# Optimization experiments

Hardware: AMD Instinct MI355X
Metric: run time of the kernel (lower is better)

Reference implementation:

```python
import jax, jax.numpy as jnp
import numpy as np

VOCAB = 100000
EMB = 100
HID = 100
CTX_LEN = 60          # must equal MAX_DESC_LEN for linear_1 to fit
FACT_LEN = 20
DESC_LEN = 60


def setup_inputs() -> dict:
    key = jax.random.key(0)
    ks = jax.random.split(key, 12)
    s = 0.05
    context = jax.random.randint(ks[0], (CTX_LEN, FACT_LEN), 1, VOCAB)
    fact_lengths = jax.random.randint(ks[1], (CTX_LEN,), 1, FACT_LEN)
    description = jax.random.randint(ks[2], (DESC_LEN,), 1, VOCAB)
    emb_ctx = jax.random.normal(ks[3], (VOCAB, EMB), jnp.float32) * s
    emb_ctx = emb_ctx.at[0].set(0.0)  # padding_idx=0
    emb_dec = jax.random.normal(ks[4], (VOCAB, EMB), jnp.float32) * s
    emb_dec = emb_dec.at[0].set(0.0)
    w1 = jax.random.normal(ks[5], (HID, CTX_LEN * HID), jnp.float32) * s
    b1 = jax.random.normal(ks[6], (HID,), jnp.float32) * s
    w_ih = jax.random.normal(ks[7], (3 * HID, EMB), jnp.float32) * s
    w_hh = jax.random.normal(ks[8], (3 * HID, HID), jnp.float32) * s
    b_ih = jax.random.normal(ks[9], (3 * HID,), jnp.float32) * s
    b_hh = jax.random.normal(ks[10], (3 * HID,), jnp.float32) * s
    w_out = jax.random.normal(ks[11], (VOCAB, HID), jnp.float32) * s
    b_out = jnp.zeros((VOCAB,), jnp.float32)
    return {"context": context, "fact_lengths": fact_lengths, "description": description,
            "emb_ctx": emb_ctx, "emb_dec": emb_dec, "w1": w1, "b1": b1,
            "w_ih": w_ih, "w_hh": w_hh, "b_ih": b_ih, "b_hh": b_hh,
            "w_out": w_out, "b_out": b_out}


def _forward(context, description, emb_ctx, emb_dec, w1, b1,
             w_ih, w_hh, b_ih, b_hh, w_out, b_out):
    # ---- InputModule: embed + positional fact encoder ----
    emb = emb_ctx[context]                       # [CTX_LEN, FACT_LEN, EMB]
    slen, elen = FACT_LEN, EMB
    s = jnp.arange(slen, dtype=jnp.float32) / (slen - 1)   # [slen]
    e = jnp.arange(elen, dtype=jnp.float32) / (elen - 1)   # [elen]
    l = 1.0 - s[:, None] - e[None, :] * (1.0 - 2.0 * s[:, None])  # [slen, elen]
    facts = jnp.sum(emb * l[None], axis=1)       # [CTX_LEN, EMB]

    # ---- initial decoder hidden from flattened facts ----
    h0 = facts.reshape(1, -1) @ w1.T + b1        # [1, HID]

    x0 = emb_dec[1][None, :]                     # SOS token embedding [1, EMB]

    def step(carry, tok):
        h, x = carry
        gi = x @ w_ih.T + b_ih                   # [1, 3H]
        gh = h @ w_hh.T + b_hh
        i_r, i_z, i_n = jnp.split(gi, 3, axis=-1)
        h_r, h_z, h_n = jnp.split(gh, 3, axis=-1)
        r = jax.nn.sigmoid(i_r + h_r)
        z = jax.nn.sigmoid(i_z + h_z)
        n = jnp.tanh(i_n + r * h_n)
        h_new = (1.0 - z) * n + z * h            # [1, HID]
        logits = h_new @ w_out.T + b_out         # [1, VOCAB]
        logp = jax.nn.log_softmax(logits, axis=-1)
        loss_t = -logp[0, tok]                   # NLLLoss, batch 1
        x_next = emb_dec[tok][None, :]           # teacher forcing
        return (h_new, x_next), loss_t

    (_, _), losses = jax.lax.scan(step, (h0, x0), description)
    return jnp.sum(losses).reshape(1)            # matches torch FloatTensor([.])


def reference(context, fact_lengths, description, emb_ctx, emb_dec, w1, b1,
              w_ih, w_hh, b_ih, b_hh, w_out, b_out):
    # fact_lengths is unused by the original forward (PositionalFactEncoder ignores it)
    return _forward(context, description, emb_ctx, emb_dec, w1, b1,
                    w_ih, w_hh, b_ih, b_hh, w_out, b_out)
```

## Files before the change

kernel.cpp:

```cpp
#include <hip/hip_runtime.h>
#include <hip/hip_bf16.h>
#include <math.h>

#define VOCAB 100000
#define EMB 100
#define HID 100
#define CTX_LEN 60
#define FACT_LEN 20
#define DESC_LEN 60
#define NCHUNK (VOCAB / 16)
#define GRID_B 224
#define NWAVES_T 892
#define CPW 8

#define WS_H0    64
#define WS_GI    192
#define WS_H     18192
#define WS_MS    24256

typedef __attribute__((ext_vector_type(8))) short short8;
typedef __attribute__((ext_vector_type(4))) float f32x4;

static __device__ __forceinline__ unsigned short f2bf(float f) {
    union { float f; unsigned u; } x; x.f = f;
    unsigned r = (x.u + 0x7FFFu + ((x.u >> 16) & 1u)) >> 16;
    return (unsigned short)r;
}

static __device__ __forceinline__ void release_flag(float* ws, int idx) {
    __builtin_amdgcn_fence(__ATOMIC_RELEASE, "agent");
    __hip_atomic_store((unsigned*)ws + idx, 1u, __ATOMIC_RELAXED, __HIP_MEMORY_SCOPE_AGENT);
}
static __device__ __forceinline__ void wait_flag(const float* ws, int idx) {
    while (__hip_atomic_load((const unsigned*)ws + idx, __ATOMIC_RELAXED,
                             __HIP_MEMORY_SCOPE_AGENT) == 0u)
        __builtin_amdgcn_s_sleep(16);
    __builtin_amdgcn_fence(__ATOMIC_ACQUIRE, "agent");
}

__global__ __launch_bounds__(320) void kA(const int* __restrict__ context,
                                          const int* __restrict__ desc,
                                          const float* __restrict__ emb_ctx,
                                          const float* __restrict__ emb_dec,
                                          const float* __restrict__ w1,
                                          const float* __restrict__ b1,
                                          const float* __restrict__ w_ih,
                                          const float* __restrict__ b_ih,
                                          float* __restrict__ ws,
                                          float* __restrict__ out) {
    const int b = blockIdx.x, tid = threadIdx.x;
    if (b < 100) {
        __shared__ int toks[1200];
        __shared__ float facts[6000];
        __shared__ float red[320];
        for (int i = tid; i < 1200; i += 320) toks[i] = context[i];
        __syncthreads();
        for (int idx = tid; idx < 6000; idx += 320) {
            int fb = idx / 100, e = idx - fb * 100;
            float ef = e * (1.f / 99.f);
            float acc = 0.f;
            #pragma unroll
            for (int s = 0; s < 20; s++) {
                float sf = s * (1.f / 19.f);
                float l = 1.f - sf - ef * (1.f - 2.f * sf);
                acc = fmaf(emb_ctx[toks[fb * 20 + s] * 100 + e], l, acc);
            }
            facts[idx] = acc;
        }
        __syncthreads();
        const float* wr = w1 + b * 6000;
        float p = 0.f;
        for (int k = tid; k < 6000; k += 320) p = fmaf(facts[k], wr[k], p);
        red[tid] = p; __syncthreads();
        if (tid < 64) red[tid] += red[256 + tid];
        __syncthreads();
        for (int st = 128; st > 0; st >>= 1) {
            if (tid < st) red[tid] += red[tid + st];
            __syncthreads();
        }
        if (tid == 0) ws[WS_H0 + b] = red[0] + b1[b];
    } else {
        const int t = b - 100;
        const int tok = (t == 0) ? 1 : desc[t - 1];
        __shared__ float xs[100];
        if (tid < 100) xs[tid] = emb_dec[tok * 100 + tid];
        __syncthreads();
        if (tid < 300) {
            float p = b_ih[tid];
            const float* wr = w_ih + tid * 100;
            #pragma unroll 4
            for (int k = 0; k < 100; k++) p = fmaf(wr[k], xs[k], p);
            ws[WS_GI + t * 300 + tid] = p;
        }
        if (b == 100) {
            if (tid >= 304 && tid < 308) ((unsigned*)ws)[(tid - 304) * 16] = 0u;
            if (tid == 319) out[0] = 0.f;
        }
    }
}

__global__ __launch_bounds__(256, 1) void kB(const float* __restrict__ w_hh,
                                             const float* __restrict__ b_hh,
                                             const float* __restrict__ w_out,
                                             const float* __restrict__ b_out,
                                             float* __restrict__ ws) {
    __shared__ __align__(16) float smem[18128];
    const int b = blockIdx.x, tid = threadIdx.x;
    const int lane = tid & 63, wave = tid >> 6;
    const int q = lane >> 4, n = lane & 15;

    if (b == 0) {
        float* gi_lds = smem;
        unsigned short (*h_bf)[128] = (unsigned short (*)[128])(smem + 18000);
        const int L = lane & 31;
        const int j = wave * 32 + L;
        const bool gate_lane = (lane < 32) && (j < 100);

        short8 bfr[3][2][4];
        #pragma unroll
        for (int s = 0; s < 3; s++) {
            #pragma unroll
            for (int c = 0; c < 2; c++) {
                const int jrow = wave * 32 + c * 16 + n;
                const float* wr = w_hh + (s * 100 + jrow) * 100;
                #pragma unroll
                for (int kt = 0; kt < 4; kt++) {
                    int k0 = kt * 32 + q * 8;
                    float va[8];
                    #pragma unroll
                    for (int jj = 0; jj < 8; jj++) va[jj] = 0.f;
                    if (jrow < 100) {
                        if (k0 + 4 <= 100) {
                            float4 a = *(const float4*)(wr + k0);
                            va[0] = a.x; va[1] = a.y; va[2] = a.z; va[3] = a.w;
                        }
                        if (k0 + 8 <= 100) {
                            float4 a = *(const float4*)(wr + k0 + 4);
                            va[4] = a.x; va[5] = a.y; va[6] = a.z; va[7] = a.w;
                        }
                    }
                    short8 f;
                    #pragma unroll
                    for (int jj = 0; jj < 8; jj++) f[jj] = (short)f2bf(va[jj]);
                    bfr[s][c][kt] = f;
                }
            }
        }

        {
            const float4* src = (const float4*)(ws + WS_GI);
            float4* dst = (float4*)gi_lds;
            for (int k = tid; k < 4500; k += 256) dst[k] = src[k];
        }

        float hreg = 0.f, bh0 = 0.f, bh1 = 0.f, bh2 = 0.f;
        if (gate_lane) {
            hreg = ws[WS_H0 + j];
            bh0 = b_hh[j]; bh1 = b_hh[100 + j]; bh2 = b_hh[200 + j];
        }
        if (tid < 128) {
            h_bf[0][tid] = (tid < 100) ? f2bf(ws[WS_H0 + tid]) : (unsigned short)0;
            h_bf[1][tid] = 0;
        }
        __syncthreads();

        const int js = (j < 100) ? j : 0;
        for (int t = 0; t < 60; t++) {
            const int rb = t & 1;
            float gir = gi_lds[t * 300 + js];
            float giz = gi_lds[t * 300 + 100 + js];
            float gin = gi_lds[t * 300 + 200 + js];

            short8 afr[4];
            #pragma unroll
            for (int kt = 0; kt < 4; kt++)
                afr[kt] = *(const short8*)&h_bf[rb][kt * 32 + q * 8];

            f32x4 acc[3][2];
            #pragma unroll
            for (int s = 0; s < 3; s++) {
                #pragma unroll
                for (int c = 0; c < 2; c++) {
                    f32x4 a = {0.f, 0.f, 0.f, 0.f};
                    a = __builtin_amdgcn_mfma_f32_16x16x32_bf16(afr[0], bfr[s][c][0], a, 0, 0, 0);
                    a = __builtin_amdgcn_mfma_f32_16x16x32_bf16(afr[1], bfr[s][c][1], a, 0, 0, 0);
                    a = __builtin_amdgcn_mfma_f32_16x16x32_bf16(afr[2], bfr[s][c][2], a, 0, 0, 0);
                    a = __builtin_amdgcn_mfma_f32_16x16x32_bf16(afr[3], bfr[s][c][3], a, 0, 0, 0);
                    acc[s][c] = a;
                }
            }

            if (gate_lane) {
                const int cc = L >> 4;
                float ghr = (cc ? acc[0][1][0] : acc[0][0][0]) + bh0;
                float ghz = (cc ? acc[1][1][0] : acc[1][0][0]) + bh1;
                float ghn = (cc ? acc[2][1][0] : acc[2][0][0]) + bh2;
                float r = 1.f / (1.f + __expf(-(gir + ghr)));
                float z = 1.f / (1.f + __expf(-(giz + ghz)));
                float a2 = fmaf(r, ghn, gin);
                float tt = __expf(-2.f * fabsf(a2));
                float nn = copysignf((1.f - tt) / (1.f + tt), a2);
                hreg = (1.f - z) * nn + z * hreg;
                h_bf[rb ^ 1][j] = f2bf(hreg);
                ws[WS_H + t * 100 + j] = hreg;
            }
            __syncthreads();
            if (t == 15 || t == 31 || t == 47 || t == 59) {
                if (tid == 0) release_flag(ws, (t >> 4) * 16);
            }
        }
        return;
    }

    const int gw = (b - 1) * 4 + wave;
    short8 bw[CPW][4];
    #pragma unroll
    for (int k = 0; k < CPW; k++) {
        int c = gw + k * NWAVES_T;
        if (c < NCHUNK) {
            const float* wr = w_out + (c * 16 + n) * 100;
            #pragma unroll
            for (int kt = 0; kt < 4; kt++) {
                int k0 = kt * 32 + q * 8;
                float va[8];
                #pragma unroll
                for (int jj = 0; jj < 8; jj++) va[jj] = 0.f;
                if (k0 + 4 <= 100) {
                    float4 a = *(const float4*)(wr + k0);
                    va[0] = a.x; va[1] = a.y; va[2] = a.z; va[3] = a.w;
                }
                if (k0 + 8 <= 100) {
                    float4 a = *(const float4*)(wr + k0 + 4);
                    va[4] = a.x; va[5] = a.y; va[6] = a.z; va[7] = a.w;
                }
                short8 f;
                #pragma unroll
                for (int jj = 0; jj < 8; jj++) f[jj] = (short)f2bf(va[jj]);
                bw[k][kt] = f;
            }
        }
    }

    const float* H = ws + WS_H;
    const int k_base = q * 8;
    float mS[16], sS[16];
    #pragma unroll
    for (int i = 0; i < 16; i++) { mS[i] = -3.0e38f; sS[i] = 0.f; }

    #pragma unroll
    for (int p = 0; p < 4; p++) {
        if (tid == 0) wait_flag(ws, p * 16);
        __syncthreads();

        short8 afr[4];
        const int m = p * 16 + n;
        #pragma unroll
        for (int kt = 0; kt < 4; kt++) {
            int k0 = kt * 32 + k_base;
            float va[8];
            #pragma unroll
            for (int jj = 0; jj < 8; jj++) va[jj] = 0.f;
            if (m < 60) {
                if (k0 + 4 <= 100) {
                    float4 a = *(const float4*)(H + m * 100 + k0);
                    va[0] = a.x; va[1] = a.y; va[2] = a.z; va[3] = a.w;
                }
                if (k0 + 8 <= 100) {
                    float4 a = *(const float4*)(H + m * 100 + k0 + 4);
                    va[4] = a.x; va[5] = a.y; va[6] = a.z; va[7] = a.w;
                }
            }
            short8 f;
            #pragma unroll
            for (int jj = 0; jj < 8; jj++) f[jj] = (short)f2bf(va[jj]);
            afr[kt] = f;
        }

        #pragma unroll
        for (int k = 0; k < CPW; k++) {
            int c = gw + k * NWAVES_T;
            if (c < NCHUNK) {
                int row = c * 16 + n;
                float bo = b_out[row];
                f32x4 acc = {0.f, 0.f, 0.f, 0.f};
                acc = __builtin_amdgcn_mfma_f32_16x16x32_bf16(afr[0], bw[k][0], acc, 0, 0, 0);
                acc = __builtin_amdgcn_mfma_f32_16x16x32_bf16(afr[1], bw[k][1], acc, 0, 0, 0);
                acc = __builtin_amdgcn_mfma_f32_16x16x32_bf16(afr[2], bw[k][2], acc, 0, 0, 0);
                acc = __builtin_amdgcn_mfma_f32_16x16x32_bf16(afr[3], bw[k][3], acc, 0, 0, 0);
                #pragma unroll
                for (int reg = 0; reg < 4; reg++) {
                    float x = acc[reg] + bo;
                    const int i = p * 4 + reg;
                    float mo = mS[i];
                    float mn = fmaxf(mo, x);
                    sS[i] = sS[i] * __expf(mo - mn) + __expf(x - mn);
                    mS[i] = mn;
                }
            }
        }
    }

    #pragma unroll
    for (int i = 0; i < 16; i++) {
        float m = mS[i], s = sS[i];
        #pragma unroll
        for (int off = 1; off < 16; off <<= 1) {
            float m2 = __shfl_xor(m, off);
            float s2 = __shfl_xor(s, off);
            float mn = fmaxf(m, m2);
            s = s * __expf(m - mn) + s2 * __expf(m2 - mn);
            m = mn;
        }
        mS[i] = m; sS[i] = s;
    }
    if (n == 0) {
        float* ms = ws + WS_MS;
        #pragma unroll
        for (int mt = 0; mt < 4; mt++) {
            #pragma unroll
            for (int reg = 0; reg < 4; reg++) {
                int t = mt * 16 + q * 4 + reg;
                int i = mt * 4 + reg;
                if (t < 60) {
                    float2 val; val.x = mS[i]; val.y = sS[i];
                    ((float2*)ms)[t * NWAVES_T + gw] = val;
                }
            }
        }
    }
}

__global__ __launch_bounds__(256) void kD(const int* __restrict__ desc,
                                          const float* __restrict__ w_out,
                                          const float* __restrict__ b_out,
                                          const float* __restrict__ ws,
                                          float* __restrict__ out) {
    const int t = blockIdx.x, tid = threadIdx.x;
    __shared__ float sm[256], ss[256], sd[256];
    const float2* msp = (const float2*)(ws + WS_MS);
    float m = -3.0e38f, s = 0.f;
    for (int i = tid; i < NWAVES_T; i += 256) {
        float2 p2 = msp[t * NWAVES_T + i];
        float mn = fmaxf(m, p2.x);
        s = s * __expf(m - mn) + p2.y * __expf(p2.x - mn);
        m = mn;
    }
    sm[tid] = m; ss[tid] = s; __syncthreads();
    for (int st = 128; st > 0; st >>= 1) {
        if (tid < st) {
            float mo = sm[tid], so = ss[tid];
            float m2 = sm[tid + st], s2 = ss[tid + st];
            float mn = fmaxf(mo, m2);
            sm[tid] = mn;
            ss[tid] = so * __expf(mo - mn) + s2 * __expf(m2 - mn);
        }
        __syncthreads();
    }
    const int tok = desc[t];
    float p = 0.f;
    if (tid < 100) p = ws[WS_H + t * 100 + tid] * w_out[tok * 100 + tid];
    sd[tid] = p; __syncthreads();
    for (int st = 128; st > 0; st >>= 1) {
        if (tid < st) sd[tid] += sd[tid + st];
        __syncthreads();
    }
    if (tid == 0) {
        float logit = sd[0] + b_out[tok];
        atomicAdd(out, sm[0] + logf(ss[0]) - logit);
    }
}

extern "C" void kernel_launch(void* const* d_in, const int* in_sizes, int n_in,
                              void* d_out, int out_size, void* d_ws, size_t ws_size,
                              hipStream_t stream) {
    const int*   context = (const int*)d_in[0];
    const int*   desc    = (const int*)d_in[2];
    const float* emb_ctx = (const float*)d_in[3];
    const float* emb_dec = (const float*)d_in[4];
    const float* w1      = (const float*)d_in[5];
    const float* b1      = (const float*)d_in[6];
    const float* w_ih    = (const float*)d_in[7];
    const float* w_hh    = (const float*)d_in[8];
    const float* b_ih    = (const float*)d_in[9];
    const float* b_hh    = (const float*)d_in[10];
    const float* w_out   = (const float*)d_in[11];
    const float* b_out   = (const float*)d_in[12];
    float* out = (float*)d_out;
    float* ws  = (float*)d_ws;

    kA<<<160, 320, 0, stream>>>(context, desc, emb_ctx, emb_dec, w1, b1, w_ih, b_ih, ws, out);
    kB<<<GRID_B, 256, 0, stream>>>(w_hh, b_hh, w_out, b_out, ws);
    kD<<<60, 256, 0, stream>>>(desc, w_out, b_out, ws, out);
}
```

Before: 201.9 us.

## Fuse final log-softmax reduction kernel into kB using per-block completion flags

```diff
diff --git a/kernel.cpp b/kernel.cpp
--- a/kernel.cpp
+++ b/kernel.cpp
@@ -13,10 +13,10 @@
 #define NWAVES_T 892
 #define CPW 8
 
-#define WS_H0    64
-#define WS_GI    192
-#define WS_H     18192
-#define WS_MS    24256
+#define WS_H0    3648
+#define WS_GI    3776
+#define WS_H     21776
+#define WS_MS    27840
 
 typedef __attribute__((ext_vector_type(8))) short short8;
 typedef __attribute__((ext_vector_type(4))) float f32x4;
@@ -93,17 +93,19 @@
             ws[WS_GI + t * 300 + tid] = p;
         }
         if (b == 100) {
-            if (tid >= 304 && tid < 308) ((unsigned*)ws)[(tid - 304) * 16] = 0u;
+            if (tid < 227) ((unsigned*)ws)[tid * 16] = 0u;
             if (tid == 319) out[0] = 0.f;
         }
     }
 }
 
-__global__ __launch_bounds__(256, 1) void kB(const float* __restrict__ w_hh,
+__global__ __launch_bounds__(256, 1) void kB(const int* __restrict__ desc,
+                                             const float* __restrict__ w_hh,
                                              const float* __restrict__ b_hh,
                                              const float* __restrict__ w_out,
                                              const float* __restrict__ b_out,
-                                             float* __restrict__ ws) {
+                                             float* __restrict__ ws,
+                                             float* __restrict__ out) {
     __shared__ __align__(16) float smem[18128];
     const int b = blockIdx.x, tid = threadIdx.x;
     const int lane = tid & 63, wave = tid >> 6;
@@ -328,45 +330,55 @@
             }
         }
     }
-}
-
-__global__ __launch_bounds__(256) void kD(const int* __restrict__ desc,
-                                          const float* __restrict__ w_out,
-                                          const float* __restrict__ b_out,
-                                          const float* __restrict__ ws,
-                                          float* __restrict__ out) {
-    const int t = blockIdx.x, tid = threadIdx.x;
-    __shared__ float sm[256], ss[256], sd[256];
-    const float2* msp = (const float2*)(ws + WS_MS);
-    float m = -3.0e38f, s = 0.f;
-    for (int i = tid; i < NWAVES_T; i += 256) {
-        float2 p2 = msp[t * NWAVES_T + i];
-        float mn = fmaxf(m, p2.x);
-        s = s * __expf(m - mn) + p2.y * __expf(p2.x - mn);
-        m = mn;
-    }
-    sm[tid] = m; ss[tid] = s; __syncthreads();
-    for (int st = 128; st > 0; st >>= 1) {
-        if (tid < st) {
-            float mo = sm[tid], so = ss[tid];
-            float m2 = sm[tid + st], s2 = ss[tid + st];
-            float mn = fmaxf(mo, m2);
-            sm[tid] = mn;
-            ss[tid] = so * __expf(mo - mn) + s2 * __expf(m2 - mn);
-        }
-        __syncthreads();
-    }
-    const int tok = desc[t];
-    float p = 0.f;
-    if (tid < 100) p = ws[WS_H + t * 100 + tid] * w_out[tok * 100 + tid];
-    sd[tid] = p; __syncthreads();
-    for (int st = 128; st > 0; st >>= 1) {
-        if (tid < st) sd[tid] += sd[tid + st];
-        __syncthreads();
-    }
-    if (tid == 0) {
-        float logit = sd[0] + b_out[tok];
-        atomicAdd(out, sm[0] + logf(ss[0]) - logit);
+    __syncthreads();
+    if (tid == 0) release_flag(ws, (3 + b) * 16);
+
+    if (b > 60) return;
+
+    {
+        if (tid < 223) {
+            const unsigned* f = (const unsigned*)ws + (4 + tid) * 16;
+            while (__hip_atomic_load(f, __ATOMIC_RELAXED, __HIP_MEMORY_SCOPE_AGENT) == 0u)
+                __builtin_amdgcn_s_sleep(16);
+        }
+        __syncthreads();
+        __builtin_amdgcn_fence(__ATOMIC_ACQUIRE, "agent");
+
+        const int t = b - 1;
+        float* sm = smem;
+        float* ss = smem + 256;
+        float* sd = smem + 512;
+        const float2* msp = (const float2*)(ws + WS_MS);
+        float m = -3.0e38f, s = 0.f;
+        for (int i = tid; i < NWAVES_T; i += 256) {
+            float2 p2 = msp[t * NWAVES_T + i];
+            float mn = fmaxf(m, p2.x);
+            s = s * __expf(m - mn) + p2.y * __expf(p2.x - mn);
+            m = mn;
+        }
+        sm[tid] = m; ss[tid] = s; __syncthreads();
+        for (int st = 128; st > 0; st >>= 1) {
+            if (tid < st) {
+                float mo = sm[tid], so = ss[tid];
+                float m2 = sm[tid + st], s2 = ss[tid + st];
+                float mn = fmaxf(mo, m2);
+                sm[tid] = mn;
+                ss[tid] = so * __expf(mo - mn) + s2 * __expf(m2 - mn);
+            }
+            __syncthreads();
+        }
+        const int tok = desc[t];
+        float p = 0.f;
+        if (tid < 100) p = ws[WS_H + t * 100 + tid] * w_out[tok * 100 + tid];
+        sd[tid] = p; __syncthreads();
+        for (int st = 128; st > 0; st >>= 1) {
+            if (tid < st) sd[tid] += sd[tid + st];
+            __syncthreads();
+        }
+        if (tid == 0) {
+            float logit = sd[0] + b_out[tok];
+            atomicAdd(out, sm[0] + logf(ss[0]) - logit);
+        }
     }
 }
 
@@ -389,6 +401,5 @@
     float* ws  = (float*)d_ws;
 
     kA<<<160, 320, 0, stream>>>(context, desc, emb_ctx, emb_dec, w1, b1, w_ih, b_ih, ws, out);
-    kB<<<GRID_B, 256, 0, stream>>>(w_hh, b_hh, w_out, b_out, ws);
-    kD<<<60, 256, 0, stream>>>(desc, w_out, b_out, ws, out);
-}
+    kB<<<GRID_B, 256, 0, stream>>>(desc, w_hh, b_hh, w_out, b_out, ws, out);
+}
```

After: 207.4 us. 2.7% more time.
